# Optimization experiments

Hardware: AMD Instinct MI355X
Metric: run time of the kernel (lower is better)

## Reference

```python
import jax, jax.numpy as jnp
import numpy as np

EPS = 1e-5
DIL = 1
PAD = 1
STRIDE = 1

def conv2d(x, w, stride=1, pad=1, dil=1):
    return jax.lax.conv_general_dilated(x, w, (stride, stride), [(pad, pad), (pad, pad)],
                                        rhs_dilation=(dil, dil),
                                        dimension_numbers=('NCHW', 'OIHW', 'NCHW'))

def batchnorm(x, g, b, m, v):
    inv = g / jnp.sqrt(v + EPS)
    return x * inv[None, :, None, None] + (b - m * inv)[None, :, None, None]

def _bilinear(img, y, x):
    # img: [C,H,W]; y,x: [Ho,Wo] float sample coords; zero padding outside.
    H, W = img.shape[1], img.shape[2]
    y0 = jnp.floor(y); x0 = jnp.floor(x)
    ty = y - y0; tx = x - x0
    y0i = y0.astype(jnp.int32); x0i = x0.astype(jnp.int32)
    def g(yi, xi):
        valid = (yi >= 0) & (yi < H) & (xi >= 0) & (xi < W)
        v = img[:, jnp.clip(yi, 0, H - 1), jnp.clip(xi, 0, W - 1)]  # [C,Ho,Wo]
        return jnp.where(valid[None], v, jnp.zeros((), img.dtype))
    return (g(y0i, x0i) * ((1 - ty) * (1 - tx))[None]
            + g(y0i, x0i + 1) * ((1 - ty) * tx)[None]
            + g(y0i + 1, x0i) * (ty * (1 - tx))[None]
            + g(y0i + 1, x0i + 1) * (ty * tx)[None])

def deform_conv(x, w, offset, stride=1, pad=1, dil=1):
    # offset: [B, 18, Ho, Wo], channels 0:9 = dy per kernel tap (row-major), 9:18 = dx.
    B, C, H, W = x.shape
    Co = w.shape[0]
    Ho = (H + 2 * pad - dil * 2 - 1) // stride + 1
    Wo = (W + 2 * pad - dil * 2 - 1) // stride + 1
    off = offset.reshape(B, 2, 9, Ho, Wo)
    iy = (jnp.arange(Ho) * stride - pad).astype(x.dtype)
    ix = (jnp.arange(Wo) * stride - pad).astype(x.dtype)
    wk = w.reshape(Co, C, 9)
    out = jnp.zeros((B, Co, Ho, Wo), x.dtype)
    for k in range(9):  # fixed 3x3 kernel taps
        ky, kx = k // 3, k % 3
        ys = iy[:, None] + ky * dil + off[:, 0, k]  # [B,Ho,Wo]
        xs = ix[None, :] + kx * dil + off[:, 1, k]
        val = jax.vmap(_bilinear)(x, ys, xs)        # [B,C,Ho,Wo]
        out = out + jnp.einsum('bchw,oc->bohw', val, wk[:, :, k])
    return out

def offset_bias(dil, dtype):
    bw = jnp.array([[-1., 0., 1.]] * 3, dtype) * (dil - 1)
    bh = bw.T
    return jnp.concatenate([bh.reshape(-1), bw.reshape(-1)])  # [18]

def setup_inputs() -> dict:
    key = jax.random.key(0)
    ks = jax.random.split(key, 12)
    B, C, H, W = 8, 256, 56, 56
    inp = {
        'x': jax.random.normal(ks[0], (B, C, H, W), jnp.float32),
        'conv1_w': jax.random.normal(ks[1], (C, C, 3, 3), jnp.float32) * 0.02,
        'bn1_g': jax.random.normal(ks[2], (C,), jnp.float32) * 0.1 + 1.0,
        'bn1_b': jax.random.normal(ks[3], (C,), jnp.float32) * 0.1,
        'bn1_m': jax.random.normal(ks[4], (C,), jnp.float32) * 0.1,
        'bn1_v': jax.random.uniform(ks[5], (C,), jnp.float32) + 0.5,
        'off_w': jax.random.normal(ks[6], (18, C, 3, 3), jnp.float32) * 0.01,
        'off_b': jnp.zeros((18,), jnp.float32),
        'conv2_w': jax.random.normal(ks[7], (C, C, 3, 3), jnp.float32) * 0.02,
        'bn2_g': jax.random.normal(ks[8], (C,), jnp.float32) * 0.1 + 1.0,
        'bn2_b': jax.random.normal(ks[9], (C,), jnp.float32) * 0.1,
        'bn2_m': jax.random.normal(ks[10], (C,), jnp.float32) * 0.1,
        'bn2_v': jax.random.uniform(ks[11], (C,), jnp.float32) + 0.5,
    }
    return inp

def reference(x, conv1_w, bn1_g, bn1_b, bn1_m, bn1_v, off_w, off_b, conv2_w, bn2_g, bn2_b, bn2_m, bn2_v):
    residual = x
    out = conv2d(x, conv1_w, STRIDE, PAD, DIL)
    out = jax.nn.relu(batchnorm(out, bn1_g, bn1_b, bn1_m, bn1_v))
    offset = conv2d(out, off_w, STRIDE, PAD, DIL) + off_b[None, :, None, None]
    offset = offset + offset_bias(DIL, out.dtype)[None, :, None, None]
    out = deform_conv(out, conv2_w, offset, STRIDE, PAD, DIL)
    out = batchnorm(out, bn2_g, bn2_b, bn2_m, bn2_v)
    return jax.nn.relu(out + residual)
```

## Files before the change

kernel.cpp:

```cpp
#include <hip/hip_runtime.h>

#define NB 8
#define NH 56
#define NW 56
#define NHW 3136
#define NCHW 802816
#define NPIX 25088
#define NHP 58
#define EPSV 1e-5f

typedef float f32x4 __attribute__((ext_vector_type(4)));
typedef __bf16 bf16x8 __attribute__((ext_vector_type(8)));

__device__ __forceinline__ unsigned short f2b(float f) {
  unsigned int u = __float_as_uint(f);
  u += 0x7FFFu + ((u >> 16) & 1u);
  return (unsigned short)(u >> 16);
}
__device__ __forceinline__ float blo(unsigned int u){ return __uint_as_float(u << 16); }
__device__ __forceinline__ float bhi(unsigned int u){ return __uint_as_float(u & 0xFFFF0000u); }
__device__ __forceinline__ unsigned int pack_trunc(float f0, float f1) {
  return __builtin_amdgcn_perm(__float_as_uint(f1), __float_as_uint(f0), 0x07060302u);
}
__device__ __forceinline__ void soft_barrier() {
  __builtin_amdgcn_s_waitcnt(0xC07F);
  __builtin_amdgcn_s_barrier();
}

__global__ __launch_bounds__(256) void clear_borders(
    unsigned short* __restrict__ xbp, unsigned short* __restrict__ t1b)
{
  int i = blockIdx.x*256 + threadIdx.x;
  int q = i & 31; int pid = i >> 5;
  int b = pid / 228, j = pid % 228;
  int y, x;
  if (j < 58)       { y = 0;  x = j; }
  else if (j < 116) { y = 57; x = j - 58; }
  else { int jj = j - 116; y = 1 + (jj >> 1); x = (jj & 1) * 57; }
  size_t addr = ((size_t)(b*NHP + y)*NHP + x)*256 + q*8;
  uint4 z = make_uint4(0u,0u,0u,0u);
  *(uint4*)(xbp + addr) = z;
  *(uint4*)(t1b + addr) = z;
}

__global__ __launch_bounds__(256) void prep_x(
    const float* __restrict__ x, unsigned short* __restrict__ xbp)
{
  __shared__ float T[64][65];
  const int pxt  = blockIdx.x * 64;
  const int cg   = blockIdx.y * 64;
  const int b    = pxt / NHW;
  const int rem0 = pxt % NHW;
  const int t    = threadIdx.x;
  const int pl   = t & 63;
  const int c0   = t >> 6;
  const float* src = x + (size_t)b*NCHW + rem0;
  #pragma unroll
  for (int it = 0; it < 16; ++it) {
    int c = c0 + it*4;
    T[c][pl] = src[(size_t)(cg + c)*NHW + pl];
  }
  __syncthreads();
  const int pr = t >> 5;
  const int cp = t & 31;
  #pragma unroll
  for (int it = 0; it < 8; ++it) {
    int pxl = pr + it*8;
    int rem = rem0 + pxl;
    int ho = rem / NW, wo = rem % NW;
    unsigned int pk = ((unsigned int)f2b(T[cp*2+1][pxl]) << 16) | (unsigned int)f2b(T[cp*2][pxl]);
    *(unsigned int*)(xbp + ((size_t)(b*NHP + ho + 1)*NHP + (wo + 1))*256 + cg + cp*2) = pk;
  }
}

__global__ __launch_bounds__(256) void prep_w(
    const float* __restrict__ w, unsigned short* __restrict__ wp)
{
  int i = blockIdx.x*256 + threadIdx.x;
  int co = i / 2304;
  int r  = i % 2304;
  int k  = r >> 8;
  int ci = r & 255;
  wp[i] = f2b(w[((size_t)co*256 + ci)*9 + k]);
}

__global__ __launch_bounds__(256) void prep_w3(
    const float* __restrict__ ow, unsigned short* __restrict__ w3p)
{
  int i = blockIdx.x*256 + threadIdx.x;
  int co = i / 2304;
  int r  = i % 2304;
  int k  = r >> 8;
  int ci = r & 255;
  w3p[i] = (co < 18) ? f2b(ow[((size_t)co*256 + ci)*9 + k]) : (unsigned short)0;
}

__global__ __launch_bounds__(512, 4) void gemm_conv1(
    const unsigned short* __restrict__ xbp, const unsigned short* __restrict__ w1p,
    const float* __restrict__ gam, const float* __restrict__ bet,
    const float* __restrict__ mu,  const float* __restrict__ var,
    unsigned short* __restrict__ t1b)
{
  __shared__ unsigned short SMEM[20480];
  unsigned short* Al = SMEM;
  unsigned short* Bl = SMEM + 4096;

  const int m0   = blockIdx.x * 64;
  const int t    = threadIdx.x;
  const int lane = t & 63;
  const int wv   = t >> 6;
  const int wvM  = wv & 1;
  const int wvN  = wv >> 1;
  const int quad = lane >> 4;
  const int l15  = lane & 15;

  const int srow = t >> 3;
  const int seg  = t & 7;
  const int sxor = srow & 7;
  const int px  = m0 + srow;
  const int b   = px / NHW, rem = px % NHW;
  const int ho  = rem / NW, wo = rem % NW;
  const unsigned int pbase = ((unsigned int)(b*NHP + ho)*NHP + wo)*256u + seg*8u;

  f32x4 acc[2][4];
  #pragma unroll
  for (int i = 0; i < 2; ++i)
    #pragma unroll
    for (int j = 0; j < 4; ++j) acc[i][j] = (f32x4)(0.f);

  uint4 pA, pB0, pB1, pB2, pB3;
  {
    pA  = *(const uint4*)(xbp + pbase);
    const unsigned int rb = seg*8u;
    pB0 = *(const uint4*)(w1p + (size_t)(srow      )*2304 + rb);
    pB1 = *(const uint4*)(w1p + (size_t)(srow +  64)*2304 + rb);
    pB2 = *(const uint4*)(w1p + (size_t)(srow + 128)*2304 + rb);
    pB3 = *(const uint4*)(w1p + (size_t)(srow + 192)*2304 + rb);
  }

  for (int r = 0; r < 36; ++r) {
    __syncthreads();
    *(uint4*)(&Al[srow*64 + ((seg ^ sxor)*8)]) = pA;
    *(uint4*)(&Bl[(srow      )*64 + ((seg ^ sxor)*8)]) = pB0;
    *(uint4*)(&Bl[(srow +  64)*64 + ((seg ^ sxor)*8)]) = pB1;
    *(uint4*)(&Bl[(srow + 128)*64 + ((seg ^ sxor)*8)]) = pB2;
    *(uint4*)(&Bl[(srow + 192)*64 + ((seg ^ sxor)*8)]) = pB3;
    {
      const int rn = (r < 35) ? r + 1 : 35;
      const int kn = rn >> 2, cicn = rn & 3;
      const int kyn = kn/3, kxn = kn - kyn*3;
      pA  = *(const uint4*)(xbp + pbase + (unsigned int)((kyn*NHP + kxn)*256 + cicn*64));
      const unsigned int rb = (unsigned int)(rn*64) + seg*8u;
      pB0 = *(const uint4*)(w1p + (size_t)(srow      )*2304 + rb);
      pB1 = *(const uint4*)(w1p + (size_t)(srow +  64)*2304 + rb);
      pB2 = *(const uint4*)(w1p + (size_t)(srow + 128)*2304 + rb);
      pB3 = *(const uint4*)(w1p + (size_t)(srow + 192)*2304 + rb);
    }
    soft_barrier();
    #pragma unroll
    for (int kk = 0; kk < 2; ++kk) {
      const int s8 = (kk*4 + quad) ^ (l15 & 7);
      bf16x8 af[2], bfr[4];
      #pragma unroll
      for (int mt = 0; mt < 2; ++mt)
        af[mt] = *(const bf16x8*)(&Al[(wvM*32 + mt*16 + l15)*64 + s8*8]);
      #pragma unroll
      for (int nt = 0; nt < 4; ++nt)
        bfr[nt] = *(const bf16x8*)(&Bl[(wvN*64 + nt*16 + l15)*64 + s8*8]);
      #pragma unroll
      for (int mt = 0; mt < 2; ++mt)
        #pragma unroll
        for (int nt = 0; nt < 4; ++nt)
          acc[mt][nt] = __builtin_amdgcn_mfma_f32_16x16x32_bf16(af[mt], bfr[nt], acc[mt][nt], 0, 0, 0);
    }
  }

  __syncthreads();
  unsigned short* Sw = SMEM + wv*2304;
  #pragma unroll
  for (int nt = 0; nt < 4; ++nt) {
    const int co = wvN*64 + nt*16 + l15;
    const float inv  = gam[co] * rsqrtf(var[co] + EPSV);
    const float beta = bet[co] - mu[co]*inv;
    #pragma unroll
    for (int mt = 0; mt < 2; ++mt) {
      #pragma unroll
      for (int rr = 0; rr < 4; ++rr) {
        const int pxl = mt*16 + quad*4 + rr;
        float val = acc[mt][nt][rr]*inv + beta;
        val = val > 0.f ? val : 0.f;
        Sw[pxl*72 + nt*16 + l15] = f2b(val);
      }
    }
  }
  #pragma unroll
  for (int i = 0; i < 4; ++i) {
    const int pxl = (lane >> 3) + 8*i;
    const int sc  = lane & 7;
    uint4 q = *(const uint4*)(&Sw[pxl*72 + sc*8]);
    const int pg = m0 + wvM*32 + pxl;
    const int bb = pg / NHW, rm = pg % NHW;
    const int hh = rm / NW, ww = rm % NW;
    *(uint4*)(t1b + ((size_t)(bb*NHP + hh + 1)*NHP + ww + 1)*256 + wvN*64 + sc*8) = q;
  }
}

__global__ __launch_bounds__(256, 8) void gemm_off(
    const unsigned short* __restrict__ t1b, const unsigned short* __restrict__ w3p,
    const float* __restrict__ ob, float* __restrict__ toff)
{
  __shared__ unsigned short Al[4096];
  __shared__ unsigned short Bl[2048];

  const int m0 = blockIdx.x * 64;
  const int kc = blockIdx.y;
  const int t    = threadIdx.x;
  const int lane = t & 63;
  const int wv   = t >> 6;
  const int quad = lane >> 4;
  const int l15  = lane & 15;

  const int arow = t >> 2;
  const int as4  = t & 3;
  const int axor = arow & 7;
  const int pxa  = m0 + arow;
  const int ba   = pxa / NHW, rema = pxa % NHW;
  const unsigned int pbase = ((unsigned int)(ba*NHP + rema/NW)*NHP + rema%NW)*256u;

  const int brow = t >> 3;
  const int bs   = t & 7;

  f32x4 acc[2];
  #pragma unroll
  for (int nt = 0; nt < 2; ++nt) {
    float init = 0.f;
    if (kc == 0) { int co = nt*16 + l15; init = (co < 18) ? ob[co] : 0.f; }
    acc[nt] = (f32x4)(init);
  }

  uint4 pA0, pA1, pB;
  {
    const int r = kc*9, k = r >> 2, cic = r & 3;
    const int ky = k/3, kx = k - ky*3;
    const unsigned int base = pbase + (unsigned int)((ky*NHP + kx)*256 + cic*64);
    pA0 = *(const uint4*)(t1b + base + as4*8);
    pA1 = *(const uint4*)(t1b + base + (as4+4)*8);
    pB  = *(const uint4*)(w3p + (size_t)brow*2304 + r*64 + bs*8);
  }

  for (int rr = 0; rr < 9; ++rr) {
    const int r = kc*9 + rr;
    __syncthreads();
    *(uint4*)(&Al[arow*64 + ((as4     ^ axor)*8)]) = pA0;
    *(uint4*)(&Al[arow*64 + (((as4+4) ^ axor)*8)]) = pA1;
    *(uint4*)(&Bl[brow*64 + ((bs ^ (brow & 7))*8)]) = pB;
    {
      const int rn = (rr < 8) ? r + 1 : r;
      const int kn = rn >> 2, cicn = rn & 3;
      const int kyn = kn/3, kxn = kn - kyn*3;
      const unsigned int base = pbase + (unsigned int)((kyn*NHP + kxn)*256 + cicn*64);
      pA0 = *(const uint4*)(t1b + base + as4*8);
      pA1 = *(const uint4*)(t1b + base + (as4+4)*8);
      pB  = *(const uint4*)(w3p + (size_t)brow*2304 + rn*64 + bs*8);
    }
    soft_barrier();
    #pragma unroll
    for (int kk = 0; kk < 2; ++kk) {
      const int s8 = (kk*4 + quad) ^ (l15 & 7);
      bf16x8 af = *(const bf16x8*)(&Al[(wv*16 + l15)*64 + s8*8]);
      #pragma unroll
      for (int nt = 0; nt < 2; ++nt) {
        bf16x8 bfr = *(const bf16x8*)(&Bl[(nt*16 + l15)*64 + s8*8]);
        acc[nt] = __builtin_amdgcn_mfma_f32_16x16x32_bf16(af, bfr, acc[nt], 0, 0, 0);
      }
    }
  }
  #pragma unroll
  for (int nt = 0; nt < 2; ++nt) {
    const int co = nt*16 + l15;
    if (co < 18) {
      #pragma unroll
      for (int rr2 = 0; rr2 < 4; ++rr2) {
        const int pg = m0 + wv*16 + quad*4 + rr2;
        const int bb = pg / NHW, rm = pg % NHW;
        atomicAdd(&toff[(size_t)bb*(18*NHW) + (size_t)co*NHW + rm], acc[nt][rr2]);
      }
    }
  }
}

__global__ __launch_bounds__(512, 4) void gemm_deform(
    const unsigned short* __restrict__ t1b, const unsigned short* __restrict__ w2p,
    const float* __restrict__ toff, const float* __restrict__ xres,
    const float* __restrict__ gam, const float* __restrict__ bet,
    const float* __restrict__ mu,  const float* __restrict__ var,
    float* __restrict__ outp)
{
  __shared__ unsigned short SMEM[20480];
  unsigned short* Al = SMEM;
  unsigned short* Bl = SMEM + 4096;

  const int m0   = blockIdx.x * 64;
  const int t    = threadIdx.x;
  const int lane = t & 63;
  const int wv   = t >> 6;
  const int wvM  = wv & 1;
  const int wvN  = wv >> 1;
  const int quad = lane >> 4;
  const int l15  = lane & 15;

  const int srow = t >> 3;
  const int seg  = t & 7;
  const int sxor = srow & 7;
  const int px   = m0 + srow;
  const int b    = px / NHW, rem = px % NHW;
  const int ho   = rem / NW, wo = rem % NW;
  const int obb  = b*(18*NHW) + rem;
  const unsigned int prowb = (unsigned int)(b*NHP);

  f32x4 acc[2][4];
  #pragma unroll
  for (int i = 0; i < 2; ++i)
    #pragma unroll
    for (int j = 0; j < 4; ++j) acc[i][j] = (f32x4)(0.f);

  unsigned int o00, o01, o10, o11;
  float w00, w01, w10, w11;
#define COORDS(KK) {                                                   \
    const int ky_ = (KK)/3, kx_ = (KK) - ky_*3;                        \
    const float offy = toff[obb + (KK)*NHW];                           \
    const float offx = toff[obb + (9+(KK))*NHW];                       \
    const float yf = (float)(ho - 1 + ky_) + offy;                     \
    const float xf = (float)(wo - 1 + kx_) + offx;                     \
    const float y0f = floorf(yf), x0f = floorf(xf);                    \
    const float ty = yf - y0f,   tx = xf - x0f;                        \
    const int y0p = (int)y0f + 1, x0p = (int)x0f + 1;                  \
    const int cy0 = min(max(y0p,   0), NHP-1);                         \
    const int cy1 = min(max(y0p+1, 0), NHP-1);                         \
    const int cx0 = min(max(x0p,   0), NHP-1);                         \
    const int cx1 = min(max(x0p+1, 0), NHP-1);                         \
    w00 = (1.f-ty)*(1.f-tx);  w01 = (1.f-ty)*tx;                       \
    w10 = ty*(1.f-tx);        w11 = ty*tx;                             \
    o00 = ((prowb + cy0)*NHP + cx0)*256u + seg*8u;                     \
    o01 = ((prowb + cy0)*NHP + cx1)*256u + seg*8u;                     \
    o10 = ((prowb + cy1)*NHP + cx0)*256u + seg*8u;                     \
    o11 = ((prowb + cy1)*NHP + cx1)*256u + seg*8u;                     \
  }

  COORDS(0);
  uint4 pc00, pc01, pc10, pc11, pB0, pB1, pB2, pB3;
  {
    pc00 = *(const uint4*)(t1b + o00);
    pc01 = *(const uint4*)(t1b + o01);
    pc10 = *(const uint4*)(t1b + o10);
    pc11 = *(const uint4*)(t1b + o11);
    const unsigned int rb = seg*8u;
    pB0 = *(const uint4*)(w2p + (size_t)(srow      )*2304 + rb);
    pB1 = *(const uint4*)(w2p + (size_t)(srow +  64)*2304 + rb);
    pB2 = *(const uint4*)(w2p + (size_t)(srow + 128)*2304 + rb);
    pB3 = *(const uint4*)(w2p + (size_t)(srow + 192)*2304 + rb);
  }

  for (int r = 0; r < 36; ++r) {
    __syncthreads();
    {
      uint4 res;
      {
        float a0 = w00*blo(pc00.x) + w01*blo(pc01.x) + w10*blo(pc10.x) + w11*blo(pc11.x);
        float a1 = w00*bhi(pc00.x) + w01*bhi(pc01.x) + w10*bhi(pc10.x) + w11*bhi(pc11.x);
        res.x = pack_trunc(a0, a1);
      }
      {
        float a0 = w00*blo(pc00.y) + w01*blo(pc01.y) + w10*blo(pc10.y) + w11*blo(pc11.y);
        float a1 = w00*bhi(pc00.y) + w01*bhi(pc01.y) + w10*bhi(pc10.y) + w11*bhi(pc11.y);
        res.y = pack_trunc(a0, a1);
      }
      {
        float a0 = w00*blo(pc00.z) + w01*blo(pc01.z) + w10*blo(pc10.z) + w11*blo(pc11.z);
        float a1 = w00*bhi(pc00.z) + w01*bhi(pc01.z) + w10*bhi(pc10.z) + w11*bhi(pc11.z);
        res.z = pack_trunc(a0, a1);
      }
      {
        float a0 = w00*blo(pc00.w) + w01*blo(pc01.w) + w10*blo(pc10.w) + w11*blo(pc11.w);
        float a1 = w00*bhi(pc00.w) + w01*bhi(pc01.w) + w10*bhi(pc10.w) + w11*bhi(pc11.w);
        res.w = pack_trunc(a0, a1);
      }
      *(uint4*)(&Al[srow*64 + ((seg ^ sxor)*8)]) = res;
    }
    *(uint4*)(&Bl[(srow      )*64 + ((seg ^ sxor)*8)]) = pB0;
    *(uint4*)(&Bl[(srow +  64)*64 + ((seg ^ sxor)*8)]) = pB1;
    *(uint4*)(&Bl[(srow + 128)*64 + ((seg ^ sxor)*8)]) = pB2;
    *(uint4*)(&Bl[(srow + 192)*64 + ((seg ^ sxor)*8)]) = pB3;
    {
      if ((r & 3) == 3 && r < 35) COORDS((r+1) >> 2);
      const int rn = (r < 35) ? r + 1 : 35;
      const unsigned int cio = (unsigned int)((rn & 3)*64);
      pc00 = *(const uint4*)(t1b + o00 + cio);
      pc01 = *(const uint4*)(t1b + o01 + cio);
      pc10 = *(const uint4*)(t1b + o10 + cio);
      pc11 = *(const uint4*)(t1b + o11 + cio);
      const unsigned int rb = (unsigned int)(rn*64) + seg*8u;
      pB0 = *(const uint4*)(w2p + (size_t)(srow      )*2304 + rb);
      pB1 = *(const uint4*)(w2p + (size_t)(srow +  64)*2304 + rb);
      pB2 = *(const uint4*)(w2p + (size_t)(srow + 128)*2304 + rb);
      pB3 = *(const uint4*)(w2p + (size_t)(srow + 192)*2304 + rb);
    }
    soft_barrier();
    #pragma unroll
    for (int kk = 0; kk < 2; ++kk) {
      const int s8 = (kk*4 + quad) ^ (l15 & 7);
      bf16x8 af[2], bfr[4];
      #pragma unroll
      for (int mt = 0; mt < 2; ++mt)
        af[mt] = *(const bf16x8*)(&Al[(wvM*32 + mt*16 + l15)*64 + s8*8]);
      #pragma unroll
      for (int nt = 0; nt < 4; ++nt)
        bfr[nt] = *(const bf16x8*)(&Bl[(wvN*64 + nt*16 + l15)*64 + s8*8]);
      #pragma unroll
      for (int mt = 0; mt < 2; ++mt)
        #pragma unroll
        for (int nt = 0; nt < 4; ++nt)
          acc[mt][nt] = __builtin_amdgcn_mfma_f32_16x16x32_bf16(af[mt], bfr[nt], acc[mt][nt], 0, 0, 0);
    }
  }
#undef COORDS

  __syncthreads();
  float* Sl = (float*)SMEM + wv*1056;
  const int pxl_r = lane & 31;
  const int csel  = lane >> 5;
  const int pg    = m0 + wvM*32 + pxl_r;
  const int bo    = pg / NHW, remo = pg % NHW;
  const size_t obase = (size_t)bo*NCHW + remo;
  #pragma unroll
  for (int h = 0; h < 2; ++h) {
    #pragma unroll
    for (int nt2 = 0; nt2 < 2; ++nt2) {
      const int nt = h*2 + nt2;
      #pragma unroll
      for (int mt = 0; mt < 2; ++mt) {
        #pragma unroll
        for (int rr = 0; rr < 4; ++rr) {
          const int pxl = mt*16 + quad*4 + rr;
          Sl[pxl*33 + nt2*16 + l15] = acc[mt][nt][rr];
        }
      }
    }
    #pragma unroll
    for (int j = 0; j < 16; ++j) {
      const int col = csel*16 + j;
      const int co  = wvN*64 + h*32 + col;
      const float inv  = gam[co] * rsqrtf(var[co] + EPSV);
      const float beta = bet[co] - mu[co]*inv;
      const size_t off = obase + (size_t)co*NHW;
      float val = Sl[pxl_r*33 + col];
      float o = val*inv + beta + xres[off];
      outp[off] = o > 0.f ? o : 0.f;
    }
  }
}

extern "C" void kernel_launch(void* const* d_in, const int* in_sizes, int n_in,
                              void* d_out, int out_size, void* d_ws, size_t ws_size,
                              hipStream_t stream) {
  const float* x   = (const float*)d_in[0];
  const float* w1  = (const float*)d_in[1];
  const float* g1  = (const float*)d_in[2];
  const float* b1  = (const float*)d_in[3];
  const float* m1  = (const float*)d_in[4];
  const float* v1  = (const float*)d_in[5];
  const float* ow  = (const float*)d_in[6];
  const float* ob  = (const float*)d_in[7];
  const float* w2  = (const float*)d_in[8];
  const float* g2  = (const float*)d_in[9];
  const float* b2  = (const float*)d_in[10];
  const float* m2  = (const float*)d_in[11];
  const float* v2  = (const float*)d_in[12];
  float* out = (float*)d_out;

  const size_t PADSZ = (size_t)NB*NHP*NHP*256;
  unsigned short* xbp = (unsigned short*)d_ws;
  unsigned short* t1b = xbp + PADSZ;
  float*          tof = (float*)(t1b + PADSZ);
  unsigned short* w1p = (unsigned short*)(tof + (size_t)NB*18*NHW);
  unsigned short* w2p = w1p + (size_t)589824;
  unsigned short* w3p = w2p + (size_t)589824;

  clear_borders<<<228, 256, 0, stream>>>(xbp, t1b);
  dim3 gp(392, 4, 1);
  prep_x<<<gp, 256, 0, stream>>>(x, xbp);
  prep_w<<<2304, 256, 0, stream>>>(w1, w1p);
  prep_w<<<2304, 256, 0, stream>>>(w2, w2p);
  prep_w3<<<288, 256, 0, stream>>>(ow, w3p);
  hipMemsetAsync(tof, 0, (size_t)NB*18*NHW*sizeof(float), stream);

  gemm_conv1<<<392, 512, 0, stream>>>(xbp, w1p, g1, b1, m1, v1, t1b);
  dim3 go(392, 4, 1);
  gemm_off<<<go, 256, 0, stream>>>(t1b, w3p, ob, tof);
  gemm_deform<<<392, 512, 0, stream>>>(t1b, w2p, tof, x, g2, b2, m2, v2, out);
}
```

Before: 254.1 us.

## Retile conv1 and deform GEMMs to 256-thread blocks with more CTAs and block swizzle

Conv1 now splits the output channels into two 128-wide halves across blockIdx.y, using 256-thread blocks with a 64x128 tile. The deform GEMM uses 32-pixel tiles with 256 threads covering all 256 channels, doubling the grid to 784 blocks. All three GEMMs remap block indices with an (bx&7)*N + bx>>3 swizzle, which changes how consecutive blocks are placed across XCDs. The aim is more CTAs to fill the CUs and better L2 locality, at the cost of redundant A-tile loads in conv1 and redundant bilinear gathers per weight byte in deform.

```diff
diff --git a/kernel.cpp b/kernel.cpp
--- a/kernel.cpp
+++ b/kernel.cpp
@@ -95,17 +95,21 @@
   w3p[i] = (co < 18) ? f2b(ow[((size_t)co*256 + ci)*9 + k]) : (unsigned short)0;
 }
 
-__global__ __launch_bounds__(512, 4) void gemm_conv1(
+__global__ __launch_bounds__(256, 4) void gemm_conv1(
     const unsigned short* __restrict__ xbp, const unsigned short* __restrict__ w1p,
     const float* __restrict__ gam, const float* __restrict__ bet,
     const float* __restrict__ mu,  const float* __restrict__ var,
     unsigned short* __restrict__ t1b)
 {
-  __shared__ unsigned short SMEM[20480];
+  __shared__ unsigned short SMEM[12288];
   unsigned short* Al = SMEM;
   unsigned short* Bl = SMEM + 4096;
 
-  const int m0   = blockIdx.x * 64;
+  const int bx   = blockIdx.x;
+  const int nbx  = (bx & 7)*49 + (bx >> 3);
+  const int m0   = nbx * 64;
+  const int n0   = blockIdx.y * 128;
+
   const int t    = threadIdx.x;
   const int lane = t & 63;
   const int wv   = t >> 6;
@@ -117,10 +121,16 @@
   const int srow = t >> 3;
   const int seg  = t & 7;
   const int sxor = srow & 7;
-  const int px  = m0 + srow;
-  const int b   = px / NHW, rem = px % NHW;
-  const int ho  = rem / NW, wo = rem % NW;
-  const unsigned int pbase = ((unsigned int)(b*NHP + ho)*NHP + wo)*256u + seg*8u;
+
+  unsigned int pbA0, pbA1;
+  {
+    int px0 = m0 + srow;
+    int b0 = px0 / NHW, rem0 = px0 % NHW;
+    pbA0 = ((unsigned int)(b0*NHP + rem0/NW)*NHP + rem0%NW)*256u + seg*8u;
+    int px1 = px0 + 32;
+    int b1 = px1 / NHW, rem1 = px1 % NHW;
+    pbA1 = ((unsigned int)(b1*NHP + rem1/NW)*NHP + rem1%NW)*256u + seg*8u;
+  }
 
   f32x4 acc[2][4];
   #pragma unroll
@@ -128,33 +138,33 @@
     #pragma unroll
     for (int j = 0; j < 4; ++j) acc[i][j] = (f32x4)(0.f);
 
-  uint4 pA, pB0, pB1, pB2, pB3;
+  uint4 pA0, pA1, pB[4];
   {
-    pA  = *(const uint4*)(xbp + pbase);
-    const unsigned int rb = seg*8u;
-    pB0 = *(const uint4*)(w1p + (size_t)(srow      )*2304 + rb);
-    pB1 = *(const uint4*)(w1p + (size_t)(srow +  64)*2304 + rb);
-    pB2 = *(const uint4*)(w1p + (size_t)(srow + 128)*2304 + rb);
-    pB3 = *(const uint4*)(w1p + (size_t)(srow + 192)*2304 + rb);
+    pA0 = *(const uint4*)(xbp + pbA0);
+    pA1 = *(const uint4*)(xbp + pbA1);
+    #pragma unroll
+    for (int i = 0; i < 4; ++i)
+      pB[i] = *(const uint4*)(w1p + (size_t)(n0 + srow + 32*i)*2304 + seg*8u);
   }
 
   for (int r = 0; r < 36; ++r) {
     __syncthreads();
-    *(uint4*)(&Al[srow*64 + ((seg ^ sxor)*8)]) = pA;
-    *(uint4*)(&Bl[(srow      )*64 + ((seg ^ sxor)*8)]) = pB0;
-    *(uint4*)(&Bl[(srow +  64)*64 + ((seg ^ sxor)*8)]) = pB1;
-    *(uint4*)(&Bl[(srow + 128)*64 + ((seg ^ sxor)*8)]) = pB2;
-    *(uint4*)(&Bl[(srow + 192)*64 + ((seg ^ sxor)*8)]) = pB3;
+    *(uint4*)(&Al[(srow     )*64 + ((seg ^ sxor)*8)]) = pA0;
+    *(uint4*)(&Al[(srow + 32)*64 + ((seg ^ sxor)*8)]) = pA1;
+    #pragma unroll
+    for (int i = 0; i < 4; ++i)
+      *(uint4*)(&Bl[(srow + 32*i)*64 + ((seg ^ sxor)*8)]) = pB[i];
     {
       const int rn = (r < 35) ? r + 1 : 35;
       const int kn = rn >> 2, cicn = rn & 3;
       const int kyn = kn/3, kxn = kn - kyn*3;
-      pA  = *(const uint4*)(xbp + pbase + (unsigned int)((kyn*NHP + kxn)*256 + cicn*64));
+      const unsigned int koff = (unsigned int)((kyn*NHP + kxn)*256 + cicn*64);
+      pA0 = *(const uint4*)(xbp + pbA0 + koff);
+      pA1 = *(const uint4*)(xbp + pbA1 + koff);
       const unsigned int rb = (unsigned int)(rn*64) + seg*8u;
-      pB0 = *(const uint4*)(w1p + (size_t)(srow      )*2304 + rb);
-      pB1 = *(const uint4*)(w1p + (size_t)(srow +  64)*2304 + rb);
-      pB2 = *(const uint4*)(w1p + (size_t)(srow + 128)*2304 + rb);
-      pB3 = *(const uint4*)(w1p + (size_t)(srow + 192)*2304 + rb);
+      #pragma unroll
+      for (int i = 0; i < 4; ++i)
+        pB[i] = *(const uint4*)(w1p + (size_t)(n0 + srow + 32*i)*2304 + rb);
     }
     soft_barrier();
     #pragma unroll
@@ -179,7 +189,7 @@
   unsigned short* Sw = SMEM + wv*2304;
   #pragma unroll
   for (int nt = 0; nt < 4; ++nt) {
-    const int co = wvN*64 + nt*16 + l15;
+    const int co = n0 + wvN*64 + nt*16 + l15;
     const float inv  = gam[co] * rsqrtf(var[co] + EPSV);
     const float beta = bet[co] - mu[co]*inv;
     #pragma unroll
@@ -201,7 +211,7 @@
     const int pg = m0 + wvM*32 + pxl;
     const int bb = pg / NHW, rm = pg % NHW;
     const int hh = rm / NW, ww = rm % NW;
-    *(uint4*)(t1b + ((size_t)(bb*NHP + hh + 1)*NHP + ww + 1)*256 + wvN*64 + sc*8) = q;
+    *(uint4*)(t1b + ((size_t)(bb*NHP + hh + 1)*NHP + ww + 1)*256 + n0 + wvN*64 + sc*8) = q;
   }
 }
 
@@ -212,7 +222,9 @@
   __shared__ unsigned short Al[4096];
   __shared__ unsigned short Bl[2048];
 
-  const int m0 = blockIdx.x * 64;
+  const int bx  = blockIdx.x;
+  const int nbx = (bx & 7)*49 + (bx >> 3);
+  const int m0  = nbx * 64;
   const int kc = blockIdx.y;
   const int t    = threadIdx.x;
   const int lane = t & 63;
@@ -289,23 +301,23 @@
   }
 }
 
-__global__ __launch_bounds__(512, 4) void gemm_deform(
+__global__ __launch_bounds__(256, 3) void gemm_deform(
     const unsigned short* __restrict__ t1b, const unsigned short* __restrict__ w2p,
     const float* __restrict__ toff, const float* __restrict__ xres,
     const float* __restrict__ gam, const float* __restrict__ bet,
     const float* __restrict__ mu,  const float* __restrict__ var,
     float* __restrict__ outp)
 {
-  __shared__ unsigned short SMEM[20480];
+  __shared__ unsigned short SMEM[18432];
   unsigned short* Al = SMEM;
-  unsigned short* Bl = SMEM + 4096;
-
-  const int m0   = blockIdx.x * 64;
+  unsigned short* Bl = SMEM + 2048;
+
+  const int bid  = blockIdx.x;
+  const int nb   = (bid & 7)*98 + (bid >> 3);
+  const int m0   = nb * 32;
   const int t    = threadIdx.x;
   const int lane = t & 63;
   const int wv   = t >> 6;
-  const int wvM  = wv & 1;
-  const int wvN  = wv >> 1;
   const int quad = lane >> 4;
   const int l15  = lane & 15;
 
@@ -348,17 +360,15 @@
   }
 
   COORDS(0);
-  uint4 pc00, pc01, pc10, pc11, pB0, pB1, pB2, pB3;
+  uint4 pc00, pc01, pc10, pc11, pB[8];
   {
     pc00 = *(const uint4*)(t1b + o00);
     pc01 = *(const uint4*)(t1b + o01);
     pc10 = *(const uint4*)(t1b + o10);
     pc11 = *(const uint4*)(t1b + o11);
-    const unsigned int rb = seg*8u;
-    pB0 = *(const uint4*)(w2p + (size_t)(srow      )*2304 + rb);
-    pB1 = *(const uint4*)(w2p + (size_t)(srow +  64)*2304 + rb);
-    pB2 = *(const uint4*)(w2p + (size_t)(srow + 128)*2304 + rb);
-    pB3 = *(const uint4*)(w2p + (size_t)(srow + 192)*2304 + rb);
+    #pragma unroll
+    for (int i = 0; i < 8; ++i)
+      pB[i] = *(const uint4*)(w2p + (size_t)(srow + 32*i)*2304 + seg*8u);
   }
 
   for (int r = 0; r < 36; ++r) {
@@ -387,10 +397,9 @@
       }
       *(uint4*)(&Al[srow*64 + ((seg ^ sxor)*8)]) = res;
     }
-    *(uint4*)(&Bl[(srow      )*64 + ((seg ^ sxor)*8)]) = pB0;
-    *(uint4*)(&Bl[(srow +  64)*64 + ((seg ^ sxor)*8)]) = pB1;
-    *(uint4*)(&Bl[(srow + 128)*64 + ((seg ^ sxor)*8)]) = pB2;
-    *(uint4*)(&Bl[(srow + 192)*64 + ((seg ^ sxor)*8)]) = pB3;
+    #pragma unroll
+    for (int i = 0; i < 8; ++i)
+      *(uint4*)(&Bl[(srow + 32*i)*64 + ((seg ^ sxor)*8)]) = pB[i];
     {
       if ((r & 3) == 3 && r < 35) COORDS((r+1) >> 2);
       const int rn = (r < 35) ? r + 1 : 35;
@@ -400,10 +409,9 @@
       pc10 = *(const uint4*)(t1b + o10 + cio);
       pc11 = *(const uint4*)(t1b + o11 + cio);
       const unsigned int rb = (unsigned int)(rn*64) + seg*8u;
-      pB0 = *(const uint4*)(w2p + (size_t)(srow      )*2304 + rb);
-      pB1 = *(const uint4*)(w2p + (size_t)(srow +  64)*2304 + rb);
-      pB2 = *(const uint4*)(w2p + (size_t)(srow + 128)*2304 + rb);
-      pB3 = *(const uint4*)(w2p + (size_t)(srow + 192)*2304 + rb);
+      #pragma unroll
+      for (int i = 0; i < 8; ++i)
+        pB[i] = *(const uint4*)(w2p + (size_t)(srow + 32*i)*2304 + rb);
     }
     soft_barrier();
     #pragma unroll
@@ -412,10 +420,10 @@
       bf16x8 af[2], bfr[4];
       #pragma unroll
       for (int mt = 0; mt < 2; ++mt)
-        af[mt] = *(const bf16x8*)(&Al[(wvM*32 + mt*16 + l15)*64 + s8*8]);
+        af[mt] = *(const bf16x8*)(&Al[(mt*16 + l15)*64 + s8*8]);
       #pragma unroll
       for (int nt = 0; nt < 4; ++nt)
-        bfr[nt] = *(const bf16x8*)(&Bl[(wvN*64 + nt*16 + l15)*64 + s8*8]);
+        bfr[nt] = *(const bf16x8*)(&Bl[(wv*64 + nt*16 + l15)*64 + s8*8]);
       #pragma unroll
       for (int mt = 0; mt < 2; ++mt)
         #pragma unroll
@@ -429,7 +437,7 @@
   float* Sl = (float*)SMEM + wv*1056;
   const int pxl_r = lane & 31;
   const int csel  = lane >> 5;
-  const int pg    = m0 + wvM*32 + pxl_r;
+  const int pg    = m0 + pxl_r;
   const int bo    = pg / NHW, remo = pg % NHW;
   const size_t obase = (size_t)bo*NCHW + remo;
   #pragma unroll
@@ -449,7 +457,7 @@
     #pragma unroll
     for (int j = 0; j < 16; ++j) {
       const int col = csel*16 + j;
-      const int co  = wvN*64 + h*32 + col;
+      const int co  = wv*64 + h*32 + col;
       const float inv  = gam[co] * rsqrtf(var[co] + EPSV);
       const float beta = bet[co] - mu[co]*inv;
       const size_t off = obase + (size_t)co*NHW;
@@ -494,8 +502,9 @@
   prep_w3<<<288, 256, 0, stream>>>(ow, w3p);
   hipMemsetAsync(tof, 0, (size_t)NB*18*NHW*sizeof(float), stream);
 
-  gemm_conv1<<<392, 512, 0, stream>>>(xbp, w1p, g1, b1, m1, v1, t1b);
+  dim3 g1d(392, 2, 1);
+  gemm_conv1<<<g1d, 256, 0, stream>>>(xbp, w1p, g1, b1, m1, v1, t1b);
   dim3 go(392, 4, 1);
   gemm_off<<<go, 256, 0, stream>>>(t1b, w3p, ob, tof);
-  gemm_deform<<<392, 512, 0, stream>>>(t1b, w2p, tof, x, g2, b2, m2, v2, out);
-}
+  gemm_deform<<<784, 256, 0, stream>>>(t1b, w2p, tof, x, g2, b2, m2, v2, out);
+}
```

Result: slower. 644.6 us (+153.7%).

## Double-buffer LDS tiles in conv GEMMs and swizzle block order

Applied to the files above, without the earlier changes.

The conv1 and deform GEMM kernels move to two LDS buffers. Each iteration writes the next K-slice while MFMAs read the current one, and global prefetch runs two slices ahead, so only one barrier per iteration remains. Block indices are also remapped with an interleaved (bx&7)*49+(bx>>3) order in three kernels, likely to spread work across XCDs or improve cache locality. The cost is doubled shared memory (80KB per block), which may lower occupancy under launch_bounds(512,4).

```diff
diff --git a/kernel.cpp b/kernel.cpp
--- a/kernel.cpp
+++ b/kernel.cpp
@@ -8,6 +8,7 @@
 #define NPIX 25088
 #define NHP 58
 #define EPSV 1e-5f
+#define BUFS 20480
 
 typedef float f32x4 __attribute__((ext_vector_type(4)));
 typedef __bf16 bf16x8 __attribute__((ext_vector_type(8)));
@@ -101,11 +102,11 @@
     const float* __restrict__ mu,  const float* __restrict__ var,
     unsigned short* __restrict__ t1b)
 {
-  __shared__ unsigned short SMEM[20480];
-  unsigned short* Al = SMEM;
-  unsigned short* Bl = SMEM + 4096;
-
-  const int m0   = blockIdx.x * 64;
+  __shared__ unsigned short SMEM[2*BUFS];
+
+  const int bx   = blockIdx.x;
+  const int nbx  = (bx & 7)*49 + (bx >> 3);
+  const int m0   = nbx * 64;
   const int t    = threadIdx.x;
   const int lane = t & 63;
   const int wv   = t >> 6;
@@ -136,17 +137,32 @@
     pB1 = *(const uint4*)(w1p + (size_t)(srow +  64)*2304 + rb);
     pB2 = *(const uint4*)(w1p + (size_t)(srow + 128)*2304 + rb);
     pB3 = *(const uint4*)(w1p + (size_t)(srow + 192)*2304 + rb);
+    *(uint4*)(&SMEM[srow*64 + ((seg ^ sxor)*8)]) = pA;
+    *(uint4*)(&SMEM[4096 + (srow      )*64 + ((seg ^ sxor)*8)]) = pB0;
+    *(uint4*)(&SMEM[4096 + (srow +  64)*64 + ((seg ^ sxor)*8)]) = pB1;
+    *(uint4*)(&SMEM[4096 + (srow + 128)*64 + ((seg ^ sxor)*8)]) = pB2;
+    *(uint4*)(&SMEM[4096 + (srow + 192)*64 + ((seg ^ sxor)*8)]) = pB3;
+    pA  = *(const uint4*)(xbp + pbase + 64u);
+    const unsigned int rb1 = 64u + seg*8u;
+    pB0 = *(const uint4*)(w1p + (size_t)(srow      )*2304 + rb1);
+    pB1 = *(const uint4*)(w1p + (size_t)(srow +  64)*2304 + rb1);
+    pB2 = *(const uint4*)(w1p + (size_t)(srow + 128)*2304 + rb1);
+    pB3 = *(const uint4*)(w1p + (size_t)(srow + 192)*2304 + rb1);
+    soft_barrier();
   }
 
   for (int r = 0; r < 36; ++r) {
-    __syncthreads();
-    *(uint4*)(&Al[srow*64 + ((seg ^ sxor)*8)]) = pA;
-    *(uint4*)(&Bl[(srow      )*64 + ((seg ^ sxor)*8)]) = pB0;
-    *(uint4*)(&Bl[(srow +  64)*64 + ((seg ^ sxor)*8)]) = pB1;
-    *(uint4*)(&Bl[(srow + 128)*64 + ((seg ^ sxor)*8)]) = pB2;
-    *(uint4*)(&Bl[(srow + 192)*64 + ((seg ^ sxor)*8)]) = pB3;
+    unsigned short* Ac = SMEM + (r & 1)*BUFS;
+    unsigned short* Bc = Ac + 4096;
+    unsigned short* An = SMEM + ((r + 1) & 1)*BUFS;
+    unsigned short* Bn = An + 4096;
+    *(uint4*)(&An[srow*64 + ((seg ^ sxor)*8)]) = pA;
+    *(uint4*)(&Bn[(srow      )*64 + ((seg ^ sxor)*8)]) = pB0;
+    *(uint4*)(&Bn[(srow +  64)*64 + ((seg ^ sxor)*8)]) = pB1;
+    *(uint4*)(&Bn[(srow + 128)*64 + ((seg ^ sxor)*8)]) = pB2;
+    *(uint4*)(&Bn[(srow + 192)*64 + ((seg ^ sxor)*8)]) = pB3;
     {
-      const int rn = (r < 35) ? r + 1 : 35;
+      const int rn = (r < 34) ? r + 2 : 35;
       const int kn = rn >> 2, cicn = rn & 3;
       const int kyn = kn/3, kxn = kn - kyn*3;
       pA  = *(const uint4*)(xbp + pbase + (unsigned int)((kyn*NHP + kxn)*256 + cicn*64));
@@ -156,23 +172,23 @@
       pB2 = *(const uint4*)(w1p + (size_t)(srow + 128)*2304 + rb);
       pB3 = *(const uint4*)(w1p + (size_t)(srow + 192)*2304 + rb);
     }
-    soft_barrier();
     #pragma unroll
     for (int kk = 0; kk < 2; ++kk) {
       const int s8 = (kk*4 + quad) ^ (l15 & 7);
       bf16x8 af[2], bfr[4];
       #pragma unroll
       for (int mt = 0; mt < 2; ++mt)
-        af[mt] = *(const bf16x8*)(&Al[(wvM*32 + mt*16 + l15)*64 + s8*8]);
+        af[mt] = *(const bf16x8*)(&Ac[(wvM*32 + mt*16 + l15)*64 + s8*8]);
       #pragma unroll
       for (int nt = 0; nt < 4; ++nt)
-        bfr[nt] = *(const bf16x8*)(&Bl[(wvN*64 + nt*16 + l15)*64 + s8*8]);
+        bfr[nt] = *(const bf16x8*)(&Bc[(wvN*64 + nt*16 + l15)*64 + s8*8]);
       #pragma unroll
       for (int mt = 0; mt < 2; ++mt)
         #pragma unroll
         for (int nt = 0; nt < 4; ++nt)
           acc[mt][nt] = __builtin_amdgcn_mfma_f32_16x16x32_bf16(af[mt], bfr[nt], acc[mt][nt], 0, 0, 0);
     }
+    soft_barrier();
   }
 
   __syncthreads();
@@ -212,7 +228,9 @@
   __shared__ unsigned short Al[4096];
   __shared__ unsigned short Bl[2048];
 
-  const int m0 = blockIdx.x * 64;
+  const int bx  = blockIdx.x;
+  const int nbx = (bx & 7)*49 + (bx >> 3);
+  const int m0  = nbx * 64;
   const int kc = blockIdx.y;
   const int t    = threadIdx.x;
   const int lane = t & 63;
@@ -296,11 +314,11 @@
     const float* __restrict__ mu,  const float* __restrict__ var,
     float* __restrict__ outp)
 {
-  __shared__ unsigned short SMEM[20480];
-  unsigned short* Al = SMEM;
-  unsigned short* Bl = SMEM + 4096;
-
-  const int m0   = blockIdx.x * 64;
+  __shared__ unsigned short SMEM[2*BUFS];
+
+  const int bid  = blockIdx.x;
+  const int nb   = (bid & 7)*49 + (bid >> 3);
+  const int m0   = nb * 64;
   const int t    = threadIdx.x;
   const int lane = t & 63;
   const int wv   = t >> 6;
@@ -347,6 +365,23 @@
     o11 = ((prowb + cy1)*NHP + cx1)*256u + seg*8u;                     \
   }
 
+#define PACK_WRITE(DST) {                                                        \
+    uint4 res;                                                                   \
+    { float a0 = w00*blo(pc00.x) + w01*blo(pc01.x) + w10*blo(pc10.x) + w11*blo(pc11.x); \
+      float a1 = w00*bhi(pc00.x) + w01*bhi(pc01.x) + w10*bhi(pc10.x) + w11*bhi(pc11.x); \
+      res.x = pack_trunc(a0, a1); }                                              \
+    { float a0 = w00*blo(pc00.y) + w01*blo(pc01.y) + w10*blo(pc10.y) + w11*blo(pc11.y); \
+      float a1 = w00*bhi(pc00.y) + w01*bhi(pc01.y) + w10*bhi(pc10.y) + w11*bhi(pc11.y); \
+      res.y = pack_trunc(a0, a1); }                                              \
+    { float a0 = w00*blo(pc00.z) + w01*blo(pc01.z) + w10*blo(pc10.z) + w11*blo(pc11.z); \
+      float a1 = w00*bhi(pc00.z) + w01*bhi(pc01.z) + w10*bhi(pc10.z) + w11*bhi(pc11.z); \
+      res.z = pack_trunc(a0, a1); }                                              \
+    { float a0 = w00*blo(pc00.w) + w01*blo(pc01.w) + w10*blo(pc10.w) + w11*blo(pc11.w); \
+      float a1 = w00*bhi(pc00.w) + w01*bhi(pc01.w) + w10*bhi(pc10.w) + w11*bhi(pc11.w); \
+      res.w = pack_trunc(a0, a1); }                                              \
+    *(uint4*)(&(DST)[srow*64 + ((seg ^ sxor)*8)]) = res;                         \
+  }
+
   COORDS(0);
   uint4 pc00, pc01, pc10, pc11, pB0, pB1, pB2, pB3;
   {
@@ -359,41 +394,36 @@
     pB1 = *(const uint4*)(w2p + (size_t)(srow +  64)*2304 + rb);
     pB2 = *(const uint4*)(w2p + (size_t)(srow + 128)*2304 + rb);
     pB3 = *(const uint4*)(w2p + (size_t)(srow + 192)*2304 + rb);
+    PACK_WRITE(SMEM);
+    *(uint4*)(&SMEM[4096 + (srow      )*64 + ((seg ^ sxor)*8)]) = pB0;
+    *(uint4*)(&SMEM[4096 + (srow +  64)*64 + ((seg ^ sxor)*8)]) = pB1;
+    *(uint4*)(&SMEM[4096 + (srow + 128)*64 + ((seg ^ sxor)*8)]) = pB2;
+    *(uint4*)(&SMEM[4096 + (srow + 192)*64 + ((seg ^ sxor)*8)]) = pB3;
+    pc00 = *(const uint4*)(t1b + o00 + 64u);
+    pc01 = *(const uint4*)(t1b + o01 + 64u);
+    pc10 = *(const uint4*)(t1b + o10 + 64u);
+    pc11 = *(const uint4*)(t1b + o11 + 64u);
+    const unsigned int rb1 = 64u + seg*8u;
+    pB0 = *(const uint4*)(w2p + (size_t)(srow      )*2304 + rb1);
+    pB1 = *(const uint4*)(w2p + (size_t)(srow +  64)*2304 + rb1);
+    pB2 = *(const uint4*)(w2p + (size_t)(srow + 128)*2304 + rb1);
+    pB3 = *(const uint4*)(w2p + (size_t)(srow + 192)*2304 + rb1);
+    soft_barrier();
   }
 
   for (int r = 0; r < 36; ++r) {
-    __syncthreads();
+    unsigned short* Ac = SMEM + (r & 1)*BUFS;
+    unsigned short* Bc = Ac + 4096;
+    unsigned short* An = SMEM + ((r + 1) & 1)*BUFS;
+    unsigned short* Bn = An + 4096;
+    PACK_WRITE(An);
+    *(uint4*)(&Bn[(srow      )*64 + ((seg ^ sxor)*8)]) = pB0;
+    *(uint4*)(&Bn[(srow +  64)*64 + ((seg ^ sxor)*8)]) = pB1;
+    *(uint4*)(&Bn[(srow + 128)*64 + ((seg ^ sxor)*8)]) = pB2;
+    *(uint4*)(&Bn[(srow + 192)*64 + ((seg ^ sxor)*8)]) = pB3;
+    if ((r & 3) == 2 && r < 34) COORDS((r + 2) >> 2);
     {
-      uint4 res;
-      {
-        float a0 = w00*blo(pc00.x) + w01*blo(pc01.x) + w10*blo(pc10.x) + w11*blo(pc11.x);
-        float a1 = w00*bhi(pc00.x) + w01*bhi(pc01.x) + w10*bhi(pc10.x) + w11*bhi(pc11.x);
-        res.x = pack_trunc(a0, a1);
-      }
-      {
-        float a0 = w00*blo(pc00.y) + w01*blo(pc01.y) + w10*blo(pc10.y) + w11*blo(pc11.y);
-        float a1 = w00*bhi(pc00.y) + w01*bhi(pc01.y) + w10*bhi(pc10.y) + w11*bhi(pc11.y);
-        res.y = pack_trunc(a0, a1);
-      }
-      {
-        float a0 = w00*blo(pc00.z) + w01*blo(pc01.z) + w10*blo(pc10.z) + w11*blo(pc11.z);
-        float a1 = w00*bhi(pc00.z) + w01*bhi(pc01.z) + w10*bhi(pc10.z) + w11*bhi(pc11.z);
-        res.z = pack_trunc(a0, a1);
-      }
-      {
-        float a0 = w00*blo(pc00.w) + w01*blo(pc01.w) + w10*blo(pc10.w) + w11*blo(pc11.w);
-        float a1 = w00*bhi(pc00.w) + w01*bhi(pc01.w) + w10*bhi(pc10.w) + w11*bhi(pc11.w);
-        res.w = pack_trunc(a0, a1);
-      }
-      *(uint4*)(&Al[srow*64 + ((seg ^ sxor)*8)]) = res;
-    }
-    *(uint4*)(&Bl[(srow      )*64 + ((seg ^ sxor)*8)]) = pB0;
-    *(uint4*)(&Bl[(srow +  64)*64 + ((seg ^ sxor)*8)]) = pB1;
-    *(uint4*)(&Bl[(srow + 128)*64 + ((seg ^ sxor)*8)]) = pB2;
-    *(uint4*)(&Bl[(srow + 192)*64 + ((seg ^ sxor)*8)]) = pB3;
-    {
-      if ((r & 3) == 3 && r < 35) COORDS((r+1) >> 2);
-      const int rn = (r < 35) ? r + 1 : 35;
+      const int rn = (r < 34) ? r + 2 : 35;
       const unsigned int cio = (unsigned int)((rn & 3)*64);
       pc00 = *(const uint4*)(t1b + o00 + cio);
       pc01 = *(const uint4*)(t1b + o01 + cio);
@@ -405,25 +435,26 @@
       pB2 = *(const uint4*)(w2p + (size_t)(srow + 128)*2304 + rb);
       pB3 = *(const uint4*)(w2p + (size_t)(srow + 192)*2304 + rb);
     }
-    soft_barrier();
     #pragma unroll
     for (int kk = 0; kk < 2; ++kk) {
       const int s8 = (kk*4 + quad) ^ (l15 & 7);
       bf16x8 af[2], bfr[4];
       #pragma unroll
       for (int mt = 0; mt < 2; ++mt)
-        af[mt] = *(const bf16x8*)(&Al[(wvM*32 + mt*16 + l15)*64 + s8*8]);
+        af[mt] = *(const bf16x8*)(&Ac[(wvM*32 + mt*16 + l15)*64 + s8*8]);
       #pragma unroll
       for (int nt = 0; nt < 4; ++nt)
-        bfr[nt] = *(const bf16x8*)(&Bl[(wvN*64 + nt*16 + l15)*64 + s8*8]);
+        bfr[nt] = *(const bf16x8*)(&Bc[(wvN*64 + nt*16 + l15)*64 + s8*8]);
       #pragma unroll
       for (int mt = 0; mt < 2; ++mt)
         #pragma unroll
         for (int nt = 0; nt < 4; ++nt)
           acc[mt][nt] = __builtin_amdgcn_mfma_f32_16x16x32_bf16(af[mt], bfr[nt], acc[mt][nt], 0, 0, 0);
     }
+    soft_barrier();
   }
 #undef COORDS
+#undef PACK_WRITE
 
   __syncthreads();
   float* Sl = (float*)SMEM + wv*1056;
```

Result: no change. 250.7 us (-1.4%).
